# Kernel optimization log

Hardware: AMD Instinct MI355X
Metric: run time of the kernel (lower is better)

The kernel has to match this reference:

```python
import jax, jax.numpy as jnp
import numpy as np

B, N, D = 16, 2048, 128  # batch, nodes, embedding_dim

def setup_inputs() -> dict:
    key = jax.random.key(0)
    ks = jax.random.split(key, 12)
    def dense(kw, kb, din, dout):
        # keras Dense default glorot_uniform weight, zeros bias (use small random bias for generality)
        lim = np.sqrt(6.0 / (din + dout))
        W = jax.random.uniform(kw, (din, dout), minval=-lim, maxval=lim, dtype=jnp.float32)
        b = jax.random.normal(kb, (dout,), dtype=jnp.float32) * 0.01
        return W, b
    Wq, bq = dense(ks[0], ks[1], D, D)
    Wk, bk = dense(ks[2], ks[3], D, D)
    Wv, bv = dense(ks[4], ks[5], D, D)
    Wo, bo = dense(ks[6], ks[7], D, D)
    query_ = jax.random.normal(ks[8], (B, N, D), dtype=jnp.float32)
    key_ = jax.random.normal(ks[9], (B, N, D), dtype=jnp.float32)
    mask = jax.random.randint(ks[10], (B, N + 1, N + 1), 0, 2).astype(bool)
    return {"query_": query_, "key_": key_, "mask": mask,
            "Wq": Wq, "bq": bq, "Wk": Wk, "bk": bk,
            "Wv": Wv, "bv": bv, "Wo": Wo, "bo": bo}

def reference(query_, key_, mask, Wq, bq, Wk, bk, Wv, bv, Wo, bo):
    q = query_ @ Wq + bq                       # [B,N,D]
    k = key_ @ Wk + bk                         # [B,N,D]
    comp = jnp.einsum('bqd,bkd->bqk', q, k)    # [B,N,N]
    comp = comp / jnp.sqrt(jnp.asarray(k.shape[-1], jnp.float32))
    m = mask[:, 1:, 1:]                        # [B,N,N]
    comp = jnp.where(m, -jnp.inf, comp)
    attn = jax.nn.softmax(comp, axis=-1)
    attn = jnp.where(jnp.isnan(attn), 0.0, attn)  # fully-masked rows -> 0
    # NOTE: faithful to source: value projection applied to the PROJECTED key
    v = k @ Wv + bv                            # [B,N,D]
    out = jnp.einsum('bqk,bkd->bqd', attn, v)
    return out @ Wo + bo
```

## Files before the change

kernel.cpp:

```cpp
#include <hip/hip_runtime.h>

#define SB 16
#define SN 2048
#define SD 128
#define NM 2049
#define SZ (SB*SN*SD)

typedef __bf16 bf16x8 __attribute__((ext_vector_type(8)));
typedef float f32x4 __attribute__((ext_vector_type(4)));

__device__ __forceinline__ unsigned short f2b(float f){
  union { float f; unsigned int u; } v; v.f = f;
  unsigned int r = v.u + 0x7fffu + ((v.u >> 16) & 1u);
  return (unsigned short)(r >> 16);
}

__device__ __forceinline__ void async16(const void* g, void* l){
  __builtin_amdgcn_global_load_lds(
      (__attribute__((address_space(1))) void*)(g),
      (__attribute__((address_space(3))) void*)(l), 16, 0, 0);
}

__global__ __launch_bounds__(256) void prep_w_kernel(
    const float* __restrict__ Wq, const float* __restrict__ Wk,
    const float* __restrict__ Wv, const float* __restrict__ Wo,
    unsigned short* __restrict__ out)
{
  int widx = blockIdx.x >> 4;
  int kg   = blockIdx.x & 15;
  const float* W = (widx==0)?Wq:(widx==1)?Wk:(widx==2)?Wv:Wo;
  unsigned short* O = out + widx*16384;
  int t = threadIdx.x;
  int k = kg*8 + (t>>5);
  int n = (t&31)*4;
  float4 v = *reinterpret_cast<const float4*>(W + k*SD + n);
  O[(n+0)*SD + k] = f2b(v.x);
  O[(n+1)*SD + k] = f2b(v.y);
  O[(n+2)*SD + k] = f2b(v.z);
  O[(n+3)*SD + k] = f2b(v.w);
}

__global__ __launch_bounds__(256) void prep_wkv_kernel(
    const float* __restrict__ Wk, const float* __restrict__ Wv,
    const float* __restrict__ bk, const float* __restrict__ bv,
    unsigned short* __restrict__ WkvT, float* __restrict__ bkv)
{
  int t = threadIdx.x;
  int k = blockIdx.x*8 + (t>>5);
  int n0 = (t&31)*4;
  float ax=0.f, ay=0.f, az=0.f, aw=0.f;
  for (int m=0;m<SD;m++){
    float wk = Wk[k*SD+m];
    float4 wv = *reinterpret_cast<const float4*>(Wv + m*SD + n0);
    ax += wk*wv.x; ay += wk*wv.y; az += wk*wv.z; aw += wk*wv.w;
  }
  WkvT[(n0+0)*SD + k] = f2b(ax);
  WkvT[(n0+1)*SD + k] = f2b(ay);
  WkvT[(n0+2)*SD + k] = f2b(az);
  WkvT[(n0+3)*SD + k] = f2b(aw);
  if (blockIdx.x==0 && t < SD){
    float a = 0.f;
    for (int m=0;m<SD;m++) a += bk[m]*Wv[m*SD + t];
    bkv[t] = a + bv[t];
  }
}

__global__ __launch_bounds__(256,4) void qkv_kernel(
    const float* __restrict__ query, const float* __restrict__ key,
    const int* __restrict__ mask,
    const unsigned short* __restrict__ wts,
    const float* __restrict__ bq, const float* __restrict__ bk,
    const float* __restrict__ bkv,
    unsigned short* __restrict__ qb, unsigned short* __restrict__ kb,
    unsigned short* __restrict__ vt, unsigned char* __restrict__ pmask8)
{
  __shared__ unsigned short vT[128*72];
  __shared__ unsigned short kq[4][16*136];

  int tid=threadIdx.x;
  int w=tid>>6, ln=tid&63, g=ln>>4, lm=ln&15;
  int bi = blockIdx.x;

  if (bi >= 1024){
    int pid = bi - 1024;
    for (int rr=0; rr<8; rr++){
      int row = pid*32 + w*8 + rr;
      int b = row >> 11, qr = row & 2047;
      const int* src = mask + (size_t)b*NM*NM + (size_t)(1+qr)*NM + 1;
      unsigned char* dst = pmask8 + (size_t)row*2048;
      for (int j=0;j<8;j++){
        int c = j*256 + ln*4;
        unsigned int pv =  (src[c+0]?1u:0u)
                        | ((src[c+1]?1u:0u)<<8)
                        | ((src[c+2]?1u:0u)<<16)
                        | ((src[c+3]?1u:0u)<<24);
        *reinterpret_cast<unsigned int*>(dst + c) = pv;
      }
    }
    return;
  }

  int id = bi >> 1;
  int b = id >> 5, nt = id & 31;
  size_t rowbase = (size_t)b*SN + nt*64 + w*16;
  unsigned short* st = &kq[w][0];
  int srow = ln>>2, sqtr = ln&3;

  if ((bi & 1) == 0){
    const unsigned short* WkT  = wts + 16384;
    const unsigned short* WkvT = wts + 32768;
    const float* xr = key + (rowbase + lm)*SD;
    bf16x8 af[4];
    for (int ks=0;ks<4;ks++){
      float4 x0 = *reinterpret_cast<const float4*>(xr + ks*32 + g*8);
      float4 x1 = *reinterpret_cast<const float4*>(xr + ks*32 + g*8 + 4);
      union { bf16x8 v; unsigned short s[8]; } u;
      u.s[0]=f2b(x0.x); u.s[1]=f2b(x0.y); u.s[2]=f2b(x0.z); u.s[3]=f2b(x0.w);
      u.s[4]=f2b(x1.x); u.s[5]=f2b(x1.y); u.s[6]=f2b(x1.z); u.s[7]=f2b(x1.w);
      af[ks]=u.v;
    }
    for (int d=0; d<8; d++){
      f32x4 acc = {0.f,0.f,0.f,0.f};
      for (int ks=0;ks<4;ks++){
        bf16x8 wf = *reinterpret_cast<const bf16x8*>(WkT + (d*16+lm)*SD + ks*32 + g*8);
        acc = __builtin_amdgcn_mfma_f32_16x16x32_bf16(af[ks], wf, acc, 0,0,0);
      }
      float bb = bk[d*16+lm];
      for (int r=0;r<4;r++)
        st[(4*g+r)*136 + d*16 + lm] = f2b(acc[r]+bb);
    }
    asm volatile("" ::: "memory");
    {
      const uint4* s4 = reinterpret_cast<const uint4*>(&st[srow*136 + sqtr*32]);
      uint4* d4 = reinterpret_cast<uint4*>(kb + (rowbase + srow)*SD + sqtr*32);
      d4[0]=s4[0]; d4[1]=s4[1]; d4[2]=s4[2]; d4[3]=s4[3];
    }
    for (int d=0; d<8; d++){
      f32x4 acc = {0.f,0.f,0.f,0.f};
      for (int ks=0;ks<4;ks++){
        bf16x8 wf = *reinterpret_cast<const bf16x8*>(WkvT + (d*16+lm)*SD + ks*32 + g*8);
        acc = __builtin_amdgcn_mfma_f32_16x16x32_bf16(wf, af[ks], acc, 0,0,0);
      }
      float4 bb = *reinterpret_cast<const float4*>(bkv + d*16 + 4*g);
      vT[(d*16 + 4*g + 0)*72 + w*16 + lm] = f2b(acc[0]+bb.x);
      vT[(d*16 + 4*g + 1)*72 + w*16 + lm] = f2b(acc[1]+bb.y);
      vT[(d*16 + 4*g + 2)*72 + w*16 + lm] = f2b(acc[2]+bb.z);
      vT[(d*16 + 4*g + 3)*72 + w*16 + lm] = f2b(acc[3]+bb.w);
    }
    __syncthreads();
    int d = tid>>1, half = tid&1;
    const uint4* src4 = reinterpret_cast<const uint4*>(&vT[d*72 + half*32]);
    uint4* dst4 = reinterpret_cast<uint4*>(vt + (size_t)b*SD*SN + (size_t)d*SN + nt*64 + half*32);
    dst4[0]=src4[0]; dst4[1]=src4[1]; dst4[2]=src4[2]; dst4[3]=src4[3];
  } else {
    const unsigned short* WqT = wts;
    const float sc = 0.08838834764831845f;
    const float* xr = query + (rowbase + lm)*SD;
    bf16x8 af[4];
    for (int ks=0;ks<4;ks++){
      float4 x0 = *reinterpret_cast<const float4*>(xr + ks*32 + g*8);
      float4 x1 = *reinterpret_cast<const float4*>(xr + ks*32 + g*8 + 4);
      union { bf16x8 v; unsigned short s[8]; } u;
      u.s[0]=f2b(x0.x); u.s[1]=f2b(x0.y); u.s[2]=f2b(x0.z); u.s[3]=f2b(x0.w);
      u.s[4]=f2b(x1.x); u.s[5]=f2b(x1.y); u.s[6]=f2b(x1.z); u.s[7]=f2b(x1.w);
      af[ks]=u.v;
    }
    for (int d=0; d<8; d++){
      f32x4 acc = {0.f,0.f,0.f,0.f};
      for (int ks=0;ks<4;ks++){
        bf16x8 wf = *reinterpret_cast<const bf16x8*>(WqT + (d*16+lm)*SD + ks*32 + g*8);
        acc = __builtin_amdgcn_mfma_f32_16x16x32_bf16(af[ks], wf, acc, 0,0,0);
      }
      float bb = bq[d*16+lm];
      for (int r=0;r<4;r++)
        st[(4*g+r)*136 + d*16 + lm] = f2b((acc[r]+bb)*sc);
    }
    asm volatile("" ::: "memory");
    {
      const uint4* s4 = reinterpret_cast<const uint4*>(&st[srow*136 + sqtr*32]);
      uint4* d4 = reinterpret_cast<uint4*>(qb + (rowbase + srow)*SD + sqtr*32);
      d4[0]=s4[0]; d4[1]=s4[1]; d4[2]=s4[2]; d4[3]=s4[3];
    }
  }
}

__global__ __launch_bounds__(256,4) void flash_kernel(
    const unsigned short* __restrict__ qb, const unsigned short* __restrict__ kb,
    const unsigned short* __restrict__ vt, const unsigned char* __restrict__ pmask8,
    const unsigned short* __restrict__ WoT, const float* __restrict__ bo,
    float* __restrict__ out)
{
  __shared__ unsigned short bufK[2][64*128];
  __shared__ unsigned short bufV[2][128*64];
  __shared__ unsigned short ldsP[4*16*72];

  int tid=threadIdx.x;
  int w=tid>>6, ln=tid&63, g=ln>>4, lm=ln&15;
  int xcd   = blockIdx.x & 7;
  int inner = blockIdx.x >> 3;
  int b  = xcd*2 + (inner>>5);
  int qt = inner & 31;
  int q0 = qt*64;

  const unsigned short* Qb = qb + (size_t)b*SN*SD;
  const unsigned short* Kb = kb + (size_t)b*SN*SD;
  const unsigned short* Vb = vt + (size_t)b*SD*SN;

  auto issueK = [&](int k0, int bi){
    const char* gbase = (const char*)Kb + (size_t)k0*256;
    for (int c=0;c<4;c++){
      int p = c*256 + tid;
      int row = p>>4, lc = (p&15) ^ (row&15);
      async16(gbase + (size_t)row*256 + lc*16, (char*)bufK[bi] + p*16);
    }
  };
  auto issueV = [&](int k0, int bi){
    const char* gbase = (const char*)Vb + (size_t)k0*2;
    for (int c=0;c<4;c++){
      int p = c*256 + tid;
      int row = p>>3, lc = (p&7) ^ (row&7);
      async16(gbase + (size_t)row*4096 + lc*16, (char*)bufV[bi] + p*16);
    }
  };

  issueK(0,0); issueV(0,0);

  bf16x8 qf[4];
  {
    const unsigned short* qr = Qb + (size_t)(q0 + w*16 + lm)*SD;
    for (int ks=0;ks<4;ks++)
      qf[ks] = *reinterpret_cast<const bf16x8*>(qr + ks*32 + g*8);
  }

  const unsigned char* pmb = pmask8 + ((size_t)(b*2048 + q0 + w*16 + 4*g))*2048 + lm;
  int mreg[16];
  for (int ct=0;ct<4;ct++)
    for (int r=0;r<4;r++)
      mreg[ct*4+r] = pmb[r*2048 + ct*16];

  float mrow[4], lrow[4], al[4];
  f32x4 acc[8];
  for (int r=0;r<4;r++){ mrow[r]=-INFINITY; lrow[r]=0.f; }
  for (int d=0;d<8;d++){ f32x4 z={0.f,0.f,0.f,0.f}; acc[d]=z; }
  unsigned short* pw = &ldsP[w*16*72];

  for (int kt=0; kt<32; kt++){
    __syncthreads();
    int cur = kt&1;
    if (kt<31){ issueK((kt+1)*64, cur^1); issueV((kt+1)*64, cur^1); }

    f32x4 s[4];
    __builtin_amdgcn_s_setprio(1);
    for (int ct=0;ct<4;ct++){
      f32x4 z = {0.f,0.f,0.f,0.f};
      for (int ks=0;ks<4;ks++){
        bf16x8 kf = *reinterpret_cast<const bf16x8*>(
            &bufK[cur][(ct*16+lm)*128 + (((ks*4+g)^lm))*8]);
        z = __builtin_amdgcn_mfma_f32_16x16x32_bf16(qf[ks], kf, z, 0,0,0);
      }
      s[ct]=z;
    }
    __builtin_amdgcn_s_setprio(0);

    for (int ct=0;ct<4;ct++)
      for (int r=0;r<4;r++)
        s[ct][r] = mreg[ct*4+r] ? -INFINITY : s[ct][r];
    if (kt<31){
      const unsigned char* mp = pmb + (kt+1)*64;
      for (int ct=0;ct<4;ct++)
        for (int r=0;r<4;r++)
          mreg[ct*4+r] = mp[r*2048 + ct*16];
    }

    for (int r=0;r<4;r++){
      float v = fmaxf(fmaxf(s[0][r],s[1][r]), fmaxf(s[2][r],s[3][r]));
      v = fmaxf(v, __shfl_xor(v,1,16));
      v = fmaxf(v, __shfl_xor(v,2,16));
      v = fmaxf(v, __shfl_xor(v,4,16));
      v = fmaxf(v, __shfl_xor(v,8,16));
      float mn = fmaxf(mrow[r], v);
      bool dead = (mn == -INFINITY);
      float a = dead ? 1.f : __expf(mrow[r]-mn);
      float rsum = 0.f;
      for (int ct=0;ct<4;ct++){
        float p = dead ? 0.f : __expf(s[ct][r]-mn);
        s[ct][r]=p; rsum += p;
      }
      rsum += __shfl_xor(rsum,1,16);
      rsum += __shfl_xor(rsum,2,16);
      rsum += __shfl_xor(rsum,4,16);
      rsum += __shfl_xor(rsum,8,16);
      lrow[r] = lrow[r]*a + rsum;
      mrow[r] = mn;
      al[r] = a;
    }
    for (int d=0;d<8;d++)
      for (int r=0;r<4;r++)
        acc[d][r] *= al[r];

    for (int ct=0;ct<4;ct++){
      int col = ct*16+lm;
      for (int r=0;r<4;r++)
        pw[(4*g+r)*72 + col] = f2b(s[ct][r]);
    }
    asm volatile("" ::: "memory");
    bf16x8 pa0 = *reinterpret_cast<const bf16x8*>(&pw[lm*72 + g*8]);
    bf16x8 pa1 = *reinterpret_cast<const bf16x8*>(&pw[lm*72 + 32 + g*8]);
    asm volatile("" ::: "memory");

    __builtin_amdgcn_s_setprio(1);
    for (int d=0;d<8;d++){
      bf16x8 v0 = *reinterpret_cast<const bf16x8*>(
          &bufV[cur][(d*16+lm)*64 + ((g^(lm&7)))*8]);
      acc[d] = __builtin_amdgcn_mfma_f32_16x16x32_bf16(pa0, v0, acc[d], 0,0,0);
      bf16x8 v1 = *reinterpret_cast<const bf16x8*>(
          &bufV[cur][(d*16+lm)*64 + (((4+g)^(lm&7)))*8]);
      acc[d] = __builtin_amdgcn_mfma_f32_16x16x32_bf16(pa1, v1, acc[d], 0,0,0);
    }
    __builtin_amdgcn_s_setprio(0);
  }

  __syncthreads();
  float inv[4];
  for (int r=0;r<4;r++) inv[r] = (lrow[r] > 0.f) ? (1.f/lrow[r]) : 0.f;
  unsigned short* strip = &bufK[0][0] + w*2176;
  for (int d=0;d<8;d++)
    for (int r=0;r<4;r++)
      strip[(4*g+r)*136 + d*16 + lm] = f2b(acc[d][r]*inv[r]);
  asm volatile("" ::: "memory");
  bf16x8 oa[4];
  for (int ks=0;ks<4;ks++)
    oa[ks] = *reinterpret_cast<const bf16x8*>(&strip[lm*136 + ks*32 + g*8]);
  asm volatile("" ::: "memory");
  float* Ob = out + ((size_t)b*SN + q0 + w*16)*SD;
  for (int dc=0; dc<8; dc++){
    f32x4 o = {0.f,0.f,0.f,0.f};
    for (int ks=0;ks<4;ks++){
      bf16x8 wf = *reinterpret_cast<const bf16x8*>(WoT + (dc*16+lm)*SD + ks*32 + g*8);
      o = __builtin_amdgcn_mfma_f32_16x16x32_bf16(oa[ks], wf, o, 0,0,0);
    }
    float bb = bo[dc*16+lm];
    for (int r=0;r<4;r++)
      __builtin_nontemporal_store(o[r]+bb, &Ob[(size_t)(4*g+r)*SD + dc*16 + lm]);
  }
}

extern "C" void kernel_launch(void* const* d_in, const int* in_sizes, int n_in,
                              void* d_out, int out_size, void* d_ws, size_t ws_size,
                              hipStream_t stream)
{
  const float* query = (const float*)d_in[0];
  const float* key   = (const float*)d_in[1];
  const int*   mask  = (const int*)d_in[2];
  const float* Wq = (const float*)d_in[3];
  const float* bq = (const float*)d_in[4];
  const float* Wk = (const float*)d_in[5];
  const float* bk = (const float*)d_in[6];
  const float* Wv = (const float*)d_in[7];
  const float* bv = (const float*)d_in[8];
  const float* Wo = (const float*)d_in[9];
  const float* bo = (const float*)d_in[10];
  float* out = (float*)d_out;

  unsigned short* qb = (unsigned short*)d_ws;
  unsigned short* kb = qb + SZ;
  unsigned short* vt = kb + SZ;
  unsigned short* wts = vt + SZ;
  float* bkv = (float*)(wts + 65536);
  unsigned char* pmask8 = (unsigned char*)(bkv + 128);

  prep_w_kernel  <<<64,256,0,stream>>>(Wq,Wk,Wv,Wo,wts);
  prep_wkv_kernel<<<16,256,0,stream>>>(Wk,Wv,bk,bv, wts+32768, bkv);
  qkv_kernel     <<<2048,256,0,stream>>>(query, key, mask, wts, bq, bk, bkv,
                                         qb, kb, vt, pmask8);
  flash_kernel   <<<512,256,0,stream>>>(qb, kb, vt, pmask8, wts+49152, bo, out);
}
```

Baseline: 537.3 us.

## Read int32 mask directly in flash kernel, drop mask prepack pass

Result: faster. 493.7 us (-8.1%).

```diff
diff --git a/kernel.cpp b/kernel.cpp
--- a/kernel.cpp
+++ b/kernel.cpp
@@ -67,12 +67,11 @@
 
 __global__ __launch_bounds__(256,4) void qkv_kernel(
     const float* __restrict__ query, const float* __restrict__ key,
-    const int* __restrict__ mask,
     const unsigned short* __restrict__ wts,
     const float* __restrict__ bq, const float* __restrict__ bk,
     const float* __restrict__ bkv,
     unsigned short* __restrict__ qb, unsigned short* __restrict__ kb,
-    unsigned short* __restrict__ vt, unsigned char* __restrict__ pmask8)
+    unsigned short* __restrict__ vt)
 {
   __shared__ unsigned short vT[128*72];
   __shared__ unsigned short kq[4][16*136];
@@ -80,25 +79,6 @@
   int tid=threadIdx.x;
   int w=tid>>6, ln=tid&63, g=ln>>4, lm=ln&15;
   int bi = blockIdx.x;
-
-  if (bi >= 1024){
-    int pid = bi - 1024;
-    for (int rr=0; rr<8; rr++){
-      int row = pid*32 + w*8 + rr;
-      int b = row >> 11, qr = row & 2047;
-      const int* src = mask + (size_t)b*NM*NM + (size_t)(1+qr)*NM + 1;
-      unsigned char* dst = pmask8 + (size_t)row*2048;
-      for (int j=0;j<8;j++){
-        int c = j*256 + ln*4;
-        unsigned int pv =  (src[c+0]?1u:0u)
-                        | ((src[c+1]?1u:0u)<<8)
-                        | ((src[c+2]?1u:0u)<<16)
-                        | ((src[c+3]?1u:0u)<<24);
-        *reinterpret_cast<unsigned int*>(dst + c) = pv;
-      }
-    }
-    return;
-  }
 
   int id = bi >> 1;
   int b = id >> 5, nt = id & 31;
@@ -186,7 +166,7 @@
 
 __global__ __launch_bounds__(256,4) void flash_kernel(
     const unsigned short* __restrict__ qb, const unsigned short* __restrict__ kb,
-    const unsigned short* __restrict__ vt, const unsigned char* __restrict__ pmask8,
+    const unsigned short* __restrict__ vt, const int* __restrict__ mask,
     const unsigned short* __restrict__ WoT, const float* __restrict__ bo,
     float* __restrict__ out)
 {
@@ -196,15 +176,13 @@
 
   int tid=threadIdx.x;
   int w=tid>>6, ln=tid&63, g=ln>>4, lm=ln&15;
-  int xcd   = blockIdx.x & 7;
-  int inner = blockIdx.x >> 3;
-  int b  = xcd*2 + (inner>>5);
-  int qt = inner & 31;
+  int b = blockIdx.x >> 5, qt = blockIdx.x & 31;
   int q0 = qt*64;
 
   const unsigned short* Qb = qb + (size_t)b*SN*SD;
   const unsigned short* Kb = kb + (size_t)b*SN*SD;
   const unsigned short* Vb = vt + (size_t)b*SD*SN;
+  const int* Mb = mask + (size_t)b*NM*NM;
 
   auto issueK = [&](int k0, int bi){
     const char* gbase = (const char*)Kb + (size_t)k0*256;
@@ -232,11 +210,12 @@
       qf[ks] = *reinterpret_cast<const bf16x8*>(qr + ks*32 + g*8);
   }
 
-  const unsigned char* pmb = pmask8 + ((size_t)(b*2048 + q0 + w*16 + 4*g))*2048 + lm;
+  int qr1 = 1 + q0 + w*16 + 4*g;
+  const int* mbase = Mb + (size_t)qr1*NM + 1 + lm;
   int mreg[16];
   for (int ct=0;ct<4;ct++)
     for (int r=0;r<4;r++)
-      mreg[ct*4+r] = pmb[r*2048 + ct*16];
+      mreg[ct*4+r] = mbase[(size_t)r*NM + ct*16];
 
   float mrow[4], lrow[4], al[4];
   f32x4 acc[8];
@@ -266,10 +245,10 @@
       for (int r=0;r<4;r++)
         s[ct][r] = mreg[ct*4+r] ? -INFINITY : s[ct][r];
     if (kt<31){
-      const unsigned char* mp = pmb + (kt+1)*64;
+      const int* mp = mbase + (kt+1)*64;
       for (int ct=0;ct<4;ct++)
         for (int r=0;r<4;r++)
-          mreg[ct*4+r] = mp[r*2048 + ct*16];
+          mreg[ct*4+r] = mp[(size_t)r*NM + ct*16];
     }
 
     for (int r=0;r<4;r++){
@@ -341,7 +320,7 @@
     }
     float bb = bo[dc*16+lm];
     for (int r=0;r<4;r++)
-      __builtin_nontemporal_store(o[r]+bb, &Ob[(size_t)(4*g+r)*SD + dc*16 + lm]);
+      Ob[(size_t)(4*g+r)*SD + dc*16 + lm] = o[r]+bb;
   }
 }
 
@@ -367,11 +346,9 @@
   unsigned short* vt = kb + SZ;
   unsigned short* wts = vt + SZ;
   float* bkv = (float*)(wts + 65536);
-  unsigned char* pmask8 = (unsigned char*)(bkv + 128);
 
   prep_w_kernel  <<<64,256,0,stream>>>(Wq,Wk,Wv,Wo,wts);
   prep_wkv_kernel<<<16,256,0,stream>>>(Wk,Wv,bk,bv, wts+32768, bkv);
-  qkv_kernel     <<<2048,256,0,stream>>>(query, key, mask, wts, bq, bk, bkv,
-                                         qb, kb, vt, pmask8);
-  flash_kernel   <<<512,256,0,stream>>>(qb, kb, vt, pmask8, wts+49152, bo, out);
-}
+  qkv_kernel     <<<1024,256,0,stream>>>(query, key, wts, bq, bk, bkv, qb, kb, vt);
+  flash_kernel   <<<512,256,0,stream>>>(qb, kb, vt, mask, wts+49152, bo, out);
+}
```
